# Performance work log

Measured on AMD Instinct MI355X. Metric: run time of the kernel, lower is better.

## Reference

```python
import jax, jax.numpy as jnp
import numpy as np

H = 32          # query heads
KV = 8          # key/value heads
HD = 128        # head_dim
EPS = 1e-6
SCALE = HD ** -0.5


def _rms_norm(x, w):
    # per-head RMSNorm over last dim in fp32
    xf = x.astype(jnp.float32)
    var = jnp.mean(xf * xf, axis=-1, keepdims=True)
    return (w * (xf * jax.lax.rsqrt(var + EPS))).astype(x.dtype)


def _rotate_half(x):
    x1, x2 = jnp.split(x, 2, axis=-1)
    return jnp.concatenate([-x2, x1], axis=-1)


def setup_inputs() -> dict:
    key = jax.random.key(0)
    ks = jax.random.split(key, 8)
    B, S, D = 1, 2048, 4096
    hidden_states = jax.random.normal(ks[0], (B, S, D), dtype=jnp.float32)
    # rotary tables (half head dim), realistic frequencies
    pos = jnp.arange(S, dtype=jnp.float32)
    inv_freq = 1.0 / (1e6 ** (jnp.arange(0, HD, 2, dtype=jnp.float32) / HD))
    ang = pos[:, None] * inv_freq[None, :]          # [S, HD/2]
    cos = jnp.broadcast_to(jnp.cos(ang)[None], (B, S, HD // 2))
    sin = jnp.broadcast_to(jnp.sin(ang)[None], (B, S, HD // 2))
    # additive causal mask [B,1,S,S]
    causal = jnp.tril(jnp.ones((S, S), dtype=bool))
    attention_mask = jnp.where(causal, 0.0, -1e9).astype(jnp.float32)[None, None]
    attention_mask = jnp.broadcast_to(attention_mask, (B, 1, S, S))
    std = 0.02
    Wq = jax.random.normal(ks[1], (H * HD, D), dtype=jnp.float32) * std
    Wk = jax.random.normal(ks[2], (KV * HD, D), dtype=jnp.float32) * std
    Wv = jax.random.normal(ks[3], (KV * HD, D), dtype=jnp.float32) * std
    Wo = jax.random.normal(ks[4], (D, H * HD), dtype=jnp.float32) * std
    q_norm_w = jnp.ones((HD,), dtype=jnp.float32)
    k_norm_w = jnp.ones((HD,), dtype=jnp.float32)
    return {"hidden_states": hidden_states, "cos": cos, "sin": sin,
            "attention_mask": attention_mask, "Wq": Wq, "Wk": Wk, "Wv": Wv,
            "Wo": Wo, "q_norm_w": q_norm_w, "k_norm_w": k_norm_w}


def reference(hidden_states, cos, sin, attention_mask, Wq, Wk, Wv, Wo, q_norm_w, k_norm_w):
    B, S, D = hidden_states.shape
    # QKV projections (no bias), reshape to heads, per-head RMSNorm on q/k
    q = (hidden_states @ Wq.T).reshape(B, S, H, HD)
    k = (hidden_states @ Wk.T).reshape(B, S, KV, HD)
    v = (hidden_states @ Wv.T).reshape(B, S, KV, HD)
    q = _rms_norm(q, q_norm_w).transpose(0, 2, 1, 3)   # [B,H,S,HD]
    k = _rms_norm(k, k_norm_w).transpose(0, 2, 1, 3)   # [B,KV,S,HD]
    v = v.transpose(0, 2, 1, 3)                        # [B,KV,S,HD]
    # RoPE: cos/sin [B,S,HD/2] -> [B,1,S,HD]
    cos2 = jnp.concatenate([cos, cos], axis=-1)[:, None]
    sin2 = jnp.concatenate([sin, sin], axis=-1)[:, None]
    q = q * cos2 + _rotate_half(q) * sin2
    k = k * cos2 + _rotate_half(k) * sin2
    # GQA repeat kv
    n_rep = H // KV
    k = jnp.repeat(k, n_rep, axis=1)                   # [B,H,S,HD]
    v = jnp.repeat(v, n_rep, axis=1)
    # eager attention, fp32 softmax
    scores = jnp.einsum('bhqd,bhkd->bhqk', q, k) * SCALE + attention_mask
    probs = jax.nn.softmax(scores.astype(jnp.float32), axis=-1).astype(q.dtype)
    attn = jnp.einsum('bhqk,bhkd->bhqd', probs, v)
    attn = attn.transpose(0, 2, 1, 3).reshape(B, S, H * HD)
    return attn @ Wo.T
```

## Files before the change

kernel.cpp:

```cpp
#include <hip/hip_runtime.h>
#include <hip/hip_bf16.h>


#define S_LEN 2048
#define D_MODEL 4096
#define NH 32
#define NKV 8
#define HD 128
#define EPS 1e-6f
#define SCALE 0.08838834764831845f
#define NEG_BIG (-1e30f)

typedef __bf16 bf16_t;
typedef __bf16 bf16x8 __attribute__((ext_vector_type(8)));
typedef __bf16 bf16x4 __attribute__((ext_vector_type(4)));
typedef float f32x4 __attribute__((ext_vector_type(4)));

__device__ __forceinline__ bool input_is_bf16(const void* qw) {
    return ((*(const unsigned*)qw) & 0xFFFFu) == 0x3F80u;
}

__device__ __forceinline__ void gload_lds16(const void* g, void* l) {
    __builtin_amdgcn_global_load_lds(
        (const __attribute__((address_space(1))) void*)g,
        (__attribute__((address_space(3))) void*)l, 16, 0, 0);
}

template<bool BF16>
__device__ __forceinline__ float ld1(const void* p, size_t i) {
    if constexpr (BF16) return (float)((const bf16_t*)p)[i];
    else return ((const float*)p)[i];
}
template<bool BF16>
__device__ __forceinline__ void st1(void* p, size_t i, float v) {
    if constexpr (BF16) ((bf16_t*)p)[i] = (bf16_t)v;
    else ((float*)p)[i] = v;
}

__device__ __forceinline__ bf16x8 cvt8(const float* src) {
    float4 a = *(const float4*)src, b = *(const float4*)(src + 4);
    bf16x8 r;
    r[0] = (bf16_t)a.x; r[1] = (bf16_t)a.y; r[2] = (bf16_t)a.z; r[3] = (bf16_t)a.w;
    r[4] = (bf16_t)b.x; r[5] = (bf16_t)b.y; r[6] = (bf16_t)b.z; r[7] = (bf16_t)b.w;
    return r;
}

__global__ __launch_bounds__(256) void conv_kernel(const void* src, const void* qw,
                                                   bf16_t* __restrict__ dst) {
    size_t i = ((size_t)blockIdx.x * 256 + threadIdx.x) * 8;
    if (input_is_bf16(qw)) {
        *(bf16x8*)&dst[i] = *(const bf16x8*)((const bf16_t*)src + i);
    } else {
        *(bf16x8*)&dst[i] = cvt8((const float*)src + i);
    }
}

__global__ __launch_bounds__(256) void convw_kernel(
    const void* Wq, const void* Wk, const void* Wv, const void* Wo,
    const void* qw, bf16_t* __restrict__ dq, bf16_t* __restrict__ dk,
    bf16_t* __restrict__ dv, bf16_t* __restrict__ dwo) {
    int b = blockIdx.x;
    const void* src; bf16_t* dst; size_t base;
    if (b < 8192)       { src = Wq; dst = dq;  base = (size_t)b * 2048; }
    else if (b < 10240) { src = Wk; dst = dk;  base = (size_t)(b - 8192) * 2048; }
    else if (b < 12288) { src = Wv; dst = dv;  base = (size_t)(b - 10240) * 2048; }
    else                { src = Wo; dst = dwo; base = (size_t)(b - 12288) * 2048; }
    size_t i = base + (size_t)threadIdx.x * 8;
    if (input_is_bf16(qw)) {
        *(bf16x8*)&dst[i] = *(const bf16x8*)((const bf16_t*)src + i);
    } else {
        *(bf16x8*)&dst[i] = cvt8((const float*)src + i);
    }
}

__device__ __forceinline__ void stage_a(const bf16_t* __restrict__ src, int m0,
                                        int k0, bf16_t* lds_a, int lane, int w) {
    #pragma unroll
    for (int i = 0; i < 2; ++i) {
        int r16 = w * 2 + i;
        gload_lds16(src + (size_t)(m0 + r16 * 16 + (lane >> 2)) * D_MODEL + k0 + (lane & 3) * 8,
                    &lds_a[r16 * 512]);
    }
}

template<bool WB>
__device__ __forceinline__ void stage_w(const void* W, size_t nrow0, int k0,
                                        bf16_t* lds_b, int tid, int lane, int w) {
    if constexpr (WB) {
        const bf16_t* Wb = (const bf16_t*)W + nrow0 * D_MODEL;
        #pragma unroll
        for (int i = 0; i < 2; ++i) {
            int r16 = w * 2 + i;
            gload_lds16(Wb + (size_t)(r16 * 16 + (lane >> 2)) * D_MODEL + k0 + (lane & 3) * 8,
                        &lds_b[r16 * 512]);
        }
    } else {
        const float* Wf = (const float*)W + nrow0 * D_MODEL;
        #pragma unroll
        for (int j = 0; j < 2; ++j) {
            int e = j * 2048 + tid * 8;
            int row = e >> 5, kk = e & 31;
            *(bf16x8*)&lds_b[e] = cvt8(Wf + (size_t)row * D_MODEL + k0 + kk);
        }
    }
}

template<bool BF16, bool WB>
__device__ void qkv_body(
    const bf16_t* __restrict__ hsb, const void* cosp, const void* sinp,
    const void* Wq, const void* Wk, const void* Wv,
    const void* qw, const void* kw,
    bf16_t* __restrict__ qn, bf16_t* __restrict__ kn, bf16_t* __restrict__ vt,
    bf16_t* lds_a, bf16_t* lds_b, int m0, int slot)
{
    const int tid = threadIdx.x;
    const int lane = tid & 63;
    const int w = tid >> 6;
    const int c = lane & 15;
    const int g = lane >> 4;

    const void* Wbase; int type, h;
    if (slot < 32)      { type = 0; h = slot;      Wbase = Wq; }
    else if (slot < 40) { type = 1; h = slot - 32; Wbase = Wk; }
    else                { type = 2; h = slot - 40; Wbase = Wv; }
    const size_t nrow0 = (size_t)h * HD;

    f32x4 acc[2][8] = {};

    stage_a(hsb, m0, 0, lds_a, lane, w);
    stage_w<WB>(Wbase, nrow0, 0, lds_b, tid, lane, w);
    __syncthreads();

    int cur = 0;
    for (int k0 = 0; k0 < D_MODEL; k0 += 32) {
        int nxt = cur ^ 1;
        if (k0 + 32 < D_MODEL) {
            stage_a(hsb, m0, k0 + 32, lds_a + nxt * 4096, lane, w);
            stage_w<WB>(Wbase, nrow0, k0 + 32, lds_b + nxt * 4096, tid, lane, w);
        }
        const bf16_t* la = lds_a + cur * 4096;
        const bf16_t* lb = lds_b + cur * 4096;
        bf16x8 af0 = *(const bf16x8*)&la[(w * 32 + c) * 32 + g * 8];
        bf16x8 af1 = *(const bf16x8*)&la[(w * 32 + 16 + c) * 32 + g * 8];
        #pragma unroll
        for (int ni = 0; ni < 8; ++ni) {
            bf16x8 bfr = *(const bf16x8*)&lb[(ni * 16 + c) * 32 + g * 8];
            acc[0][ni] = __builtin_amdgcn_mfma_f32_16x16x32_bf16(af0, bfr, acc[0][ni], 0, 0, 0);
            acc[1][ni] = __builtin_amdgcn_mfma_f32_16x16x32_bf16(af1, bfr, acc[1][ni], 0, 0, 0);
        }
        __syncthreads();
        cur = nxt;
    }

    if (type == 2) {
        #pragma unroll
        for (int mi = 0; mi < 2; ++mi) {
            int s = m0 + w * 32 + mi * 16 + g * 4;
            #pragma unroll
            for (int ni = 0; ni < 8; ++ni) {
                bf16x4 pk;
                #pragma unroll
                for (int r = 0; r < 4; ++r) pk[r] = (bf16_t)acc[mi][ni][r];
                *(bf16x4*)&vt[((size_t)h * HD + ni * 16 + c) * S_LEN + s] = pk;
            }
        }
        return;
    }

    const void* nw = (type == 0) ? qw : kw;
    bf16_t* outb = (type == 0) ? (qn + (size_t)h * S_LEN * HD)
                               : (kn + (size_t)h * S_LEN * HD);
    #pragma unroll
    for (int mi = 0; mi < 2; ++mi) {
        float ss[4];
        #pragma unroll
        for (int r = 0; r < 4; ++r) {
            float p = 0.f;
            #pragma unroll
            for (int ni = 0; ni < 8; ++ni) p += acc[mi][ni][r] * acc[mi][ni][r];
            p += __shfl_xor(p, 1); p += __shfl_xor(p, 2);
            p += __shfl_xor(p, 4); p += __shfl_xor(p, 8);
            ss[r] = rsqrtf(p * (1.f / HD) + EPS);
        }
        float v[8][4];
        #pragma unroll
        for (int ni = 0; ni < 8; ++ni) {
            float wg = ld1<BF16>(nw, ni * 16 + c);
            #pragma unroll
            for (int r = 0; r < 4; ++r) v[ni][r] = acc[mi][ni][r] * ss[r] * wg;
        }
        #pragma unroll
        for (int r = 0; r < 4; ++r) {
            int s = m0 + w * 32 + mi * 16 + g * 4 + r;
            #pragma unroll
            for (int t = 0; t < 4; ++t) {
                int nn = t * 16 + c;
                float co = ld1<BF16>(cosp, (size_t)s * 64 + nn);
                float si = ld1<BF16>(sinp, (size_t)s * 64 + nn);
                float x1 = v[t][r], x2 = v[t + 4][r];
                v[t][r]     = x1 * co - x2 * si;
                v[t + 4][r] = x2 * co + x1 * si;
            }
        }
        #pragma unroll
        for (int t = 0; t < 8; ++t)
            #pragma unroll
            for (int r = 0; r < 4; ++r) {
                int s = m0 + w * 32 + mi * 16 + g * 4 + r;
                outb[(size_t)s * HD + t * 16 + c] = (bf16_t)v[t][r];
            }
    }
}

__global__ __launch_bounds__(256) void qkv_kernel(
    const bf16_t* __restrict__ hsb, const void* cosp, const void* sinp,
    const void* Wq, const void* Wk, const void* Wv,
    const void* qw, const void* kw,
    bf16_t* __restrict__ qn, bf16_t* __restrict__ kn, bf16_t* __restrict__ vt,
    int wconv)
{
    __shared__ bf16_t lds_a[2][128 * 32];
    __shared__ bf16_t lds_b[2][128 * 32];
    const int lin = blockIdx.y * 16 + blockIdx.x;
    const int j = lin >> 3;
    const int m0   = (j & 15) * 128;
    const int slot = (lin & 7) * 6 + (j >> 4);
    bool ib = input_is_bf16(qw);
    if (wconv) {
        if (ib) qkv_body<true,  true>(hsb, cosp, sinp, Wq, Wk, Wv, qw, kw, qn, kn, vt, &lds_a[0][0], &lds_b[0][0], m0, slot);
        else    qkv_body<false, true>(hsb, cosp, sinp, Wq, Wk, Wv, qw, kw, qn, kn, vt, &lds_a[0][0], &lds_b[0][0], m0, slot);
    } else {
        if (ib) qkv_body<true,  true>(hsb, cosp, sinp, Wq, Wk, Wv, qw, kw, qn, kn, vt, &lds_a[0][0], &lds_b[0][0], m0, slot);
        else    qkv_body<false, false>(hsb, cosp, sinp, Wq, Wk, Wv, qw, kw, qn, kn, vt, &lds_a[0][0], &lds_b[0][0], m0, slot);
    }
}

__global__ __launch_bounds__(256) void attn_kernel(
    const bf16_t* __restrict__ qn, const bf16_t* __restrict__ kn,
    const bf16_t* __restrict__ vt, bf16_t* __restrict__ attnb)
{
    __shared__ bf16_t lds_k[32 * 128];
    __shared__ bf16_t lds_v[128 * 32];

    const int lane = threadIdx.x & 63;
    const int w = threadIdx.x >> 6;
    const int c = lane & 15;
    const int g = lane >> 4;
    const int lin = blockIdx.y * 16 + blockIdx.x;
    const int j = lin >> 3;
    const int xa = j & 15;
    const int h  = (lin & 7) * 4 + (j >> 4);
    const int hk = h >> 2;
    const int lr = lane >> 2;
    const int lk = (lane & 3) * 8;

    const int qrow0 = xa * 64 + w * 16;
    const int qrow1 = (31 - xa) * 64 + w * 16;
    const int kmaxA = xa * 64 + 64;
    const int kmaxB = (31 - xa) * 64 + 64;

    const bf16_t* kb_base = kn + (size_t)hk * S_LEN * HD;
    const bf16_t* vt_base = vt + (size_t)hk * HD * S_LEN;

    bf16x8 qf[2][4];
    #pragma unroll
    for (int ks = 0; ks < 4; ++ks) {
        qf[0][ks] = *(const bf16x8*)(qn + ((size_t)h * S_LEN + qrow0 + c) * HD + ks * 32 + g * 8);
        qf[1][ks] = *(const bf16x8*)(qn + ((size_t)h * S_LEN + qrow1 + c) * HD + ks * 32 + g * 8);
    }

    f32x4 o[2][8] = {};
    float m_cur[2] = {NEG_BIG, NEG_BIG};
    float l_cur[2] = {0.f, 0.f};

    for (int kb = 0; kb < kmaxB; kb += 32) {
        const bool liveA = (kb < kmaxA);
        __syncthreads();
        #pragma unroll
        for (int i = 0; i < 2; ++i) {
            int t16 = w * 2 + i;
            gload_lds16(kb_base + (size_t)(kb + t16 * 4 + g) * HD + c * 8,
                        &lds_k[t16 * 512]);
            gload_lds16(vt_base + (size_t)(t16 * 16 + lr) * S_LEN + kb + lk,
                        &lds_v[t16 * 512]);
        }
        __syncthreads();

        float p[2][2][4];
        #pragma unroll
        for (int u = 0; u < 2; ++u) {
            f32x4 sacc0 = {}, sacc1 = {};
            #pragma unroll
            for (int ks = 0; ks < 4; ++ks) {
                bf16x8 kf = *(const bf16x8*)&lds_k[(u * 16 + c) * 128 + ks * 32 + g * 8];
                if (liveA)
                    sacc0 = __builtin_amdgcn_mfma_f32_16x16x32_bf16(kf, qf[0][ks], sacc0, 0, 0, 0);
                sacc1 = __builtin_amdgcn_mfma_f32_16x16x32_bf16(kf, qf[1][ks], sacc1, 0, 0, 0);
            }
            #pragma unroll
            for (int r = 0; r < 4; ++r) {
                int key_abs = kb + u * 16 + g * 4 + r;
                p[0][u][r] = (key_abs <= qrow0 + c) ? sacc0[r] * SCALE : NEG_BIG;
                p[1][u][r] = (key_abs <= qrow1 + c) ? sacc1[r] * SCALE : NEG_BIG;
            }
        }

        bf16x8 pb[2];
        #pragma unroll
        for (int qt = 0; qt < 2; ++qt) {
            if (qt == 0 && !liveA) continue;
            float mx = NEG_BIG;
            #pragma unroll
            for (int u = 0; u < 2; ++u)
                #pragma unroll
                for (int r = 0; r < 4; ++r) mx = fmaxf(mx, p[qt][u][r]);
            mx = fmaxf(mx, __shfl_xor(mx, 16));
            mx = fmaxf(mx, __shfl_xor(mx, 32));
            float m_new = fmaxf(m_cur[qt], mx);
            float alpha = __expf(m_cur[qt] - m_new);
            float lsum = 0.f;
            #pragma unroll
            for (int u = 0; u < 2; ++u)
                #pragma unroll
                for (int r = 0; r < 4; ++r) {
                    float e = __expf(p[qt][u][r] - m_new);
                    p[qt][u][r] = e;
                    lsum += e;
                }
            lsum += __shfl_xor(lsum, 16);
            lsum += __shfl_xor(lsum, 32);
            l_cur[qt] = l_cur[qt] * alpha + lsum;
            m_cur[qt] = m_new;
            #pragma unroll
            for (int dt = 0; dt < 8; ++dt) o[qt][dt] *= alpha;
            #pragma unroll
            for (int j2 = 0; j2 < 8; ++j2) {
                int src = (((g * 2 + (j2 >> 2)) & 3) << 4) | c;
                float v0 = __shfl(p[qt][0][j2 & 3], src);
                float v1 = __shfl(p[qt][1][j2 & 3], src);
                pb[qt][j2] = (bf16_t)((g >= 2) ? v1 : v0);
            }
        }
        #pragma unroll
        for (int dt = 0; dt < 8; ++dt) {
            bf16x8 vf = *(const bf16x8*)&lds_v[(dt * 16 + c) * 32 + g * 8];
            if (liveA)
                o[0][dt] = __builtin_amdgcn_mfma_f32_16x16x32_bf16(vf, pb[0], o[0][dt], 0, 0, 0);
            o[1][dt] = __builtin_amdgcn_mfma_f32_16x16x32_bf16(vf, pb[1], o[1][dt], 0, 0, 0);
        }
    }

    #pragma unroll
    for (int qt = 0; qt < 2; ++qt) {
        float inv_l = 1.f / l_cur[qt];
        int q = (qt == 0 ? qrow0 : qrow1) + c;
        #pragma unroll
        for (int dt = 0; dt < 8; ++dt) {
            bf16x4 pk;
            #pragma unroll
            for (int r = 0; r < 4; ++r) pk[r] = (bf16_t)(o[qt][dt][r] * inv_l);
            *(bf16x4*)&attnb[(size_t)q * D_MODEL + h * HD + dt * 16 + g * 4] = pk;
        }
    }
}

template<bool BF16, bool WB>
__device__ void out_body(const bf16_t* __restrict__ attnb, const void* Wo,
                         void* outp, bf16_t* lds_a, bf16_t* lds_b,
                         int m0, int n0)
{
    const int tid = threadIdx.x;
    const int lane = tid & 63;
    const int w = tid >> 6;
    const int c = lane & 15;
    const int g = lane >> 4;
    const int wm = w >> 1, wn = w & 1;

    f32x4 acc[4][4] = {};

    stage_a(attnb, m0, 0, lds_a, lane, w);
    stage_w<WB>(Wo, (size_t)n0, 0, lds_b, tid, lane, w);
    __syncthreads();

    int cur = 0;
    for (int k0 = 0; k0 < D_MODEL; k0 += 32) {
        int nxt = cur ^ 1;
        if (k0 + 32 < D_MODEL) {
            stage_a(attnb, m0, k0 + 32, lds_a + nxt * 4096, lane, w);
            stage_w<WB>(Wo, (size_t)n0, k0 + 32, lds_b + nxt * 4096, tid, lane, w);
        }
        const bf16_t* la = lds_a + cur * 4096;
        const bf16_t* lb = lds_b + cur * 4096;
        bf16x8 af[4], bfr[4];
        #pragma unroll
        for (int i = 0; i < 4; ++i) {
            af[i]  = *(const bf16x8*)&la[(wm * 64 + i * 16 + c) * 32 + g * 8];
            bfr[i] = *(const bf16x8*)&lb[(wn * 64 + i * 16 + c) * 32 + g * 8];
        }
        #pragma unroll
        for (int mi = 0; mi < 4; ++mi)
            #pragma unroll
            for (int ni = 0; ni < 4; ++ni)
                acc[mi][ni] = __builtin_amdgcn_mfma_f32_16x16x32_bf16(af[mi], bfr[ni], acc[mi][ni], 0, 0, 0);
        __syncthreads();
        cur = nxt;
    }
    #pragma unroll
    for (int mi = 0; mi < 4; ++mi)
        #pragma unroll
        for (int ni = 0; ni < 4; ++ni)
            #pragma unroll
            for (int r = 0; r < 4; ++r)
                st1<BF16>(outp, (size_t)(m0 + wm * 64 + mi * 16 + g * 4 + r) * D_MODEL
                                 + n0 + wn * 64 + ni * 16 + c, acc[mi][ni][r]);
}

__global__ __launch_bounds__(256) void out_kernel(
    const bf16_t* __restrict__ attnb, const void* Wo, const void* qw, void* outp,
    int wconv)
{
    __shared__ bf16_t lds_a[2][128 * 32];
    __shared__ bf16_t lds_b[2][128 * 32];
    const int lin = blockIdx.y * 16 + blockIdx.x;
    const int j = lin >> 3;
    const int m0 = (j & 15) * 128;
    const int n0 = ((lin & 7) * 4 + (j >> 4)) * 128;
    bool ib = input_is_bf16(qw);
    if (wconv) {
        if (ib) out_body<true,  true>(attnb, Wo, outp, &lds_a[0][0], &lds_b[0][0], m0, n0);
        else    out_body<false, true>(attnb, Wo, outp, &lds_a[0][0], &lds_b[0][0], m0, n0);
    } else {
        if (ib) out_body<true,  true>(attnb, Wo, outp, &lds_a[0][0], &lds_b[0][0], m0, n0);
        else    out_body<false, false>(attnb, Wo, outp, &lds_a[0][0], &lds_b[0][0], m0, n0);
    }
}

extern "C" void kernel_launch(void* const* d_in, const int* in_sizes, int n_in,
                              void* d_out, int out_size, void* d_ws, size_t ws_size,
                              hipStream_t stream) {
    const void* hs   = d_in[0];
    const void* cosp = d_in[1];
    const void* sinp = d_in[2];
    const void* Wq = d_in[4];
    const void* Wk = d_in[5];
    const void* Wv = d_in[6];
    const void* Wo = d_in[7];
    const void* qw = d_in[8];
    const void* kw = d_in[9];

    const size_t NEED   = 41943040ull;
    const size_t NEED_W = NEED + 83886080ull;
    if (ws_size < NEED) return;
    const int wconv = (ws_size >= NEED_W) ? 1 : 0;

    char* ws = (char*)d_ws;
    bf16_t* buf0 = (bf16_t*)(ws);
    bf16_t* qn   = (bf16_t*)(ws + 16777216);
    bf16_t* kn   = (bf16_t*)(ws + 2 * 16777216);
    bf16_t* vt   = (bf16_t*)(ws + 2 * 16777216 + 4194304);

    conv_kernel<<<dim3(4096), 256, 0, stream>>>(hs, qw, buf0);

    if (wconv) {
        bf16_t* dq  = (bf16_t*)(ws + NEED);
        bf16_t* dk  = (bf16_t*)(ws + NEED + 33554432ull);
        bf16_t* dv  = (bf16_t*)(ws + NEED + 33554432ull + 8388608ull);
        bf16_t* dwo = (bf16_t*)(ws + NEED + 33554432ull + 2*8388608ull);
        convw_kernel<<<dim3(20480), 256, 0, stream>>>(Wq, Wk, Wv, Wo, qw, dq, dk, dv, dwo);
        qkv_kernel<<<dim3(16, 48), 256, 0, stream>>>(buf0, cosp, sinp, dq, dk, dv, qw, kw,
                                                     qn, kn, vt, 1);
        attn_kernel<<<dim3(16, 32), 256, 0, stream>>>(qn, kn, vt, buf0);
        out_kernel<<<dim3(16, 32), 256, 0, stream>>>(buf0, dwo, qw, d_out, 1);
    } else {
        qkv_kernel<<<dim3(16, 48), 256, 0, stream>>>(buf0, cosp, sinp, Wq, Wk, Wv, qw, kw,
                                                     qn, kn, vt, 0);
        attn_kernel<<<dim3(16, 32), 256, 0, stream>>>(qn, kn, vt, buf0);
        out_kernel<<<dim3(16, 32), 256, 0, stream>>>(buf0, Wo, qw, d_out, 0);
    }
}
```

Before: 675.7 us.

## Double GEMM K-tile to 64 with XOR-swizzled LDS layout

```diff
diff --git a/kernel.cpp b/kernel.cpp
--- a/kernel.cpp
+++ b/kernel.cpp
@@ -73,36 +73,34 @@
     }
 }
 
-__device__ __forceinline__ void stage_a(const bf16_t* __restrict__ src, int m0,
-                                        int k0, bf16_t* lds_a, int lane, int w) {
-    #pragma unroll
-    for (int i = 0; i < 2; ++i) {
-        int r16 = w * 2 + i;
-        gload_lds16(src + (size_t)(m0 + r16 * 16 + (lane >> 2)) * D_MODEL + k0 + (lane & 3) * 8,
-                    &lds_a[r16 * 512]);
-    }
-}
-
 template<bool WB>
-__device__ __forceinline__ void stage_w(const void* W, size_t nrow0, int k0,
-                                        bf16_t* lds_b, int tid, int lane, int w) {
+__device__ __forceinline__ void stage64(const void* W, size_t row0, int k0,
+                                        bf16_t* lds, int tid) {
+    const int t8 = tid >> 3;
+    const int cb8 = (tid & 7) * 8;
+    const int wv = tid >> 6;
     if constexpr (WB) {
-        const bf16_t* Wb = (const bf16_t*)W + nrow0 * D_MODEL;
-        #pragma unroll
-        for (int i = 0; i < 2; ++i) {
-            int r16 = w * 2 + i;
-            gload_lds16(Wb + (size_t)(r16 * 16 + (lane >> 2)) * D_MODEL + k0 + (lane & 3) * 8,
-                        &lds_b[r16 * 512]);
-        }
-    } else {
-        const float* Wf = (const float*)W + nrow0 * D_MODEL;
-        #pragma unroll
-        for (int j = 0; j < 2; ++j) {
-            int e = j * 2048 + tid * 8;
-            int row = e >> 5, kk = e & 31;
-            *(bf16x8*)&lds_b[e] = cvt8(Wf + (size_t)row * D_MODEL + k0 + kk);
-        }
-    }
+        const bf16_t* Wb = (const bf16_t*)W;
+        #pragma unroll
+        for (int i = 0; i < 4; ++i) {
+            int r = i * 32 + t8;
+            int gcol = cb8 ^ ((r & 7) << 3);
+            gload_lds16(Wb + (row0 + r) * (size_t)D_MODEL + k0 + gcol,
+                        lds + i * 2048 + wv * 512);
+        }
+    } else {
+        const float* Wf = (const float*)W;
+        #pragma unroll
+        for (int i = 0; i < 4; ++i) {
+            int r = i * 32 + t8;
+            int lcol = cb8 ^ ((r & 7) << 3);
+            *(bf16x8*)&lds[r * 64 + lcol] = cvt8(Wf + (row0 + r) * (size_t)D_MODEL + k0 + cb8);
+        }
+    }
+}
+
+__device__ __forceinline__ bf16x8 ldsw(const bf16_t* lds, int row, int colE) {
+    return *(const bf16x8*)&lds[row * 64 + (colE ^ ((row & 7) << 3))];
 }
 
 template<bool BF16, bool WB>
@@ -127,29 +125,31 @@
 
     f32x4 acc[2][8] = {};
 
-    stage_a(hsb, m0, 0, lds_a, lane, w);
-    stage_w<WB>(Wbase, nrow0, 0, lds_b, tid, lane, w);
+    stage64<WB>(hsb, (size_t)m0, 0, lds_a, tid);
+    stage64<WB>(Wbase, nrow0, 0, lds_b, tid);
     __syncthreads();
 
     int cur = 0;
-    for (int k0 = 0; k0 < D_MODEL; k0 += 32) {
-        int nxt = cur ^ 1;
-        if (k0 + 32 < D_MODEL) {
-            stage_a(hsb, m0, k0 + 32, lds_a + nxt * 4096, lane, w);
-            stage_w<WB>(Wbase, nrow0, k0 + 32, lds_b + nxt * 4096, tid, lane, w);
-        }
-        const bf16_t* la = lds_a + cur * 4096;
-        const bf16_t* lb = lds_b + cur * 4096;
-        bf16x8 af0 = *(const bf16x8*)&la[(w * 32 + c) * 32 + g * 8];
-        bf16x8 af1 = *(const bf16x8*)&la[(w * 32 + 16 + c) * 32 + g * 8];
-        #pragma unroll
-        for (int ni = 0; ni < 8; ++ni) {
-            bf16x8 bfr = *(const bf16x8*)&lb[(ni * 16 + c) * 32 + g * 8];
-            acc[0][ni] = __builtin_amdgcn_mfma_f32_16x16x32_bf16(af0, bfr, acc[0][ni], 0, 0, 0);
-            acc[1][ni] = __builtin_amdgcn_mfma_f32_16x16x32_bf16(af1, bfr, acc[1][ni], 0, 0, 0);
+    for (int it = 0; it < 64; ++it) {
+        if (it + 1 < 64) {
+            stage64<WB>(hsb, (size_t)m0, (it + 1) * 64, lds_a + (cur ^ 1) * 8192, tid);
+            stage64<WB>(Wbase, nrow0, (it + 1) * 64, lds_b + (cur ^ 1) * 8192, tid);
+        }
+        const bf16_t* la = lds_a + cur * 8192;
+        const bf16_t* lb = lds_b + cur * 8192;
+        #pragma unroll
+        for (int ks = 0; ks < 2; ++ks) {
+            bf16x8 af0 = ldsw(la, w * 32 + c, ks * 32 + g * 8);
+            bf16x8 af1 = ldsw(la, w * 32 + 16 + c, ks * 32 + g * 8);
+            #pragma unroll
+            for (int ni = 0; ni < 8; ++ni) {
+                bf16x8 bfr = ldsw(lb, ni * 16 + c, ks * 32 + g * 8);
+                acc[0][ni] = __builtin_amdgcn_mfma_f32_16x16x32_bf16(af0, bfr, acc[0][ni], 0, 0, 0);
+                acc[1][ni] = __builtin_amdgcn_mfma_f32_16x16x32_bf16(af1, bfr, acc[1][ni], 0, 0, 0);
+            }
         }
         __syncthreads();
-        cur = nxt;
+        cur ^= 1;
     }
 
     if (type == 2) {
@@ -219,8 +219,8 @@
     bf16_t* __restrict__ qn, bf16_t* __restrict__ kn, bf16_t* __restrict__ vt,
     int wconv)
 {
-    __shared__ bf16_t lds_a[2][128 * 32];
-    __shared__ bf16_t lds_b[2][128 * 32];
+    __shared__ bf16_t lds_a[2][128 * 64];
+    __shared__ bf16_t lds_b[2][128 * 64];
     const int lin = blockIdx.y * 16 + blockIdx.x;
     const int j = lin >> 3;
     const int m0   = (j & 15) * 128;
@@ -378,32 +378,34 @@
 
     f32x4 acc[4][4] = {};
 
-    stage_a(attnb, m0, 0, lds_a, lane, w);
-    stage_w<WB>(Wo, (size_t)n0, 0, lds_b, tid, lane, w);
+    stage64<WB>(attnb, (size_t)m0, 0, lds_a, tid);
+    stage64<WB>(Wo, (size_t)n0, 0, lds_b, tid);
     __syncthreads();
 
     int cur = 0;
-    for (int k0 = 0; k0 < D_MODEL; k0 += 32) {
-        int nxt = cur ^ 1;
-        if (k0 + 32 < D_MODEL) {
-            stage_a(attnb, m0, k0 + 32, lds_a + nxt * 4096, lane, w);
-            stage_w<WB>(Wo, (size_t)n0, k0 + 32, lds_b + nxt * 4096, tid, lane, w);
-        }
-        const bf16_t* la = lds_a + cur * 4096;
-        const bf16_t* lb = lds_b + cur * 4096;
-        bf16x8 af[4], bfr[4];
-        #pragma unroll
-        for (int i = 0; i < 4; ++i) {
-            af[i]  = *(const bf16x8*)&la[(wm * 64 + i * 16 + c) * 32 + g * 8];
-            bfr[i] = *(const bf16x8*)&lb[(wn * 64 + i * 16 + c) * 32 + g * 8];
-        }
-        #pragma unroll
-        for (int mi = 0; mi < 4; ++mi)
-            #pragma unroll
-            for (int ni = 0; ni < 4; ++ni)
-                acc[mi][ni] = __builtin_amdgcn_mfma_f32_16x16x32_bf16(af[mi], bfr[ni], acc[mi][ni], 0, 0, 0);
+    for (int it = 0; it < 64; ++it) {
+        if (it + 1 < 64) {
+            stage64<WB>(attnb, (size_t)m0, (it + 1) * 64, lds_a + (cur ^ 1) * 8192, tid);
+            stage64<WB>(Wo, (size_t)n0, (it + 1) * 64, lds_b + (cur ^ 1) * 8192, tid);
+        }
+        const bf16_t* la = lds_a + cur * 8192;
+        const bf16_t* lb = lds_b + cur * 8192;
+        #pragma unroll
+        for (int ks = 0; ks < 2; ++ks) {
+            bf16x8 af[4], bfr[4];
+            #pragma unroll
+            for (int i = 0; i < 4; ++i) {
+                af[i]  = ldsw(la, wm * 64 + i * 16 + c, ks * 32 + g * 8);
+                bfr[i] = ldsw(lb, wn * 64 + i * 16 + c, ks * 32 + g * 8);
+            }
+            #pragma unroll
+            for (int mi = 0; mi < 4; ++mi)
+                #pragma unroll
+                for (int ni = 0; ni < 4; ++ni)
+                    acc[mi][ni] = __builtin_amdgcn_mfma_f32_16x16x32_bf16(af[mi], bfr[ni], acc[mi][ni], 0, 0, 0);
+        }
         __syncthreads();
-        cur = nxt;
+        cur ^= 1;
     }
     #pragma unroll
     for (int mi = 0; mi < 4; ++mi)
@@ -419,8 +421,8 @@
     const bf16_t* __restrict__ attnb, const void* Wo, const void* qw, void* outp,
     int wconv)
 {
-    __shared__ bf16_t lds_a[2][128 * 32];
-    __shared__ bf16_t lds_b[2][128 * 32];
+    __shared__ bf16_t lds_a[2][128 * 64];
+    __shared__ bf16_t lds_b[2][128 * 64];
     const int lin = blockIdx.y * 16 + blockIdx.x;
     const int j = lin >> 3;
     const int m0 = (j & 15) * 128;
```

New measurement: 735.8 us. 1.09x slower.
